# Optimization experiments

Measured on AMD Instinct MI355X. Metric: run time of the kernel, lower is better.

The kernel has to match this reference:

```python
import jax, jax.numpy as jnp
import numpy as np
import math


def _fft_size(n: int) -> int:
    return max(2 * 2 ** int(math.ceil(math.log2(n))), 16)


def setup_inputs() -> dict:
    key = jax.random.key(0)
    k1, k2 = jax.random.split(key)
    b, n, d = 4, 8192, 512
    x = jax.random.normal(k1, (b, n, d), dtype=jnp.float32)
    t = jax.random.normal(k2, (n, d), dtype=jnp.float32)
    return {"x": x, "t": t}


def reference(x, t):
    # x: (b, n, d); t: (n, d) Toeplitz coefficients t0..t_{n-1} per channel.
    # o[b, i, d] = gelu( sum_{j<=i} t[i-j, d] * x[b, j, d] )
    # computed via zero-padded real FFT of size >= 2n (causal linear conv).
    b, n, d = x.shape
    N = _fft_size(n)  # 2 * next_pow2(n)
    t_f = jnp.fft.rfft(t, n=N, axis=0)          # (N//2+1, d) complex
    x_f = jnp.fft.rfft(x, n=N, axis=1)          # (b, N//2+1, d) complex
    y = jnp.fft.irfft(x_f * t_f[None], n=N, axis=1)[:, :n, :]  # (b, n, d)
    return jax.nn.gelu(y)
```

## Files before the change

kernel.cpp:

```cpp
#include <hip/hip_runtime.h>
#include <hip/hip_bf16.h>
#include <math.h>

typedef short short8 __attribute__((ext_vector_type(8)));
typedef float f32x4  __attribute__((ext_vector_type(4)));

#define N_SEQ 8192
#define D_CH  512

__device__ __forceinline__ unsigned short f32_to_bf16_bits(float f) {
    union { float f; unsigned int u; } v; v.f = f;
    unsigned int u = v.u;
    unsigned int r = u + 0x7FFFu + ((u >> 16) & 1u);
    return (unsigned short)(r >> 16);
}

__global__ __launch_bounds__(256) void transpose_cast_kernel(
    const float* __restrict__ x, const float* __restrict__ t,
    unsigned short* __restrict__ xT, unsigned short* __restrict__ tT) {
  __shared__ float tile[64][65];
  int blk = blockIdx.x;
  int bat = blk >> 10;
  int rem = blk & 1023;
  int i0 = (rem >> 3) << 6;
  int d0 = (rem & 7) << 6;
  const float* src; unsigned short* dst;
  if (bat < 4) { src = x + (size_t)bat * N_SEQ * D_CH; dst = xT + (size_t)bat * D_CH * N_SEQ; }
  else         { src = t;                              dst = tT; }
  int tx = threadIdx.x & 63, ty = threadIdx.x >> 6;
  #pragma unroll
  for (int r = ty; r < 64; r += 4)
    tile[r][tx] = src[(size_t)(i0 + r) * D_CH + (d0 + tx)];
  __syncthreads();
  #pragma unroll
  for (int r = ty; r < 64; r += 4)
    dst[(size_t)(d0 + r) * N_SEQ + (i0 + tx)] = f32_to_bf16_bits(tile[tx][r]);
}

__global__ __launch_bounds__(256) void transpose_out_kernel(
    const float* __restrict__ src, float* __restrict__ dst) {
  __shared__ float tile[64][65];
  int blk = blockIdx.x;
  int b   = blk >> 10;
  int rem = blk & 1023;
  int d0 = (rem & 7) << 6;
  int i0 = (rem >> 3) << 6;
  int tx = threadIdx.x & 63, ty = threadIdx.x >> 6;
  #pragma unroll
  for (int r = ty; r < 64; r += 4)
    tile[r][tx] = src[((size_t)(d0 + r) * 4 + b) * N_SEQ + i0 + tx];
  __syncthreads();
  #pragma unroll
  for (int r = ty; r < 64; r += 4)
    dst[((size_t)b * N_SEQ + i0 + r) * D_CH + d0 + tx] = tile[tx][r];
}

constexpr int XLDS_B   = 8192;
constexpr int TSTRIDE  = 272;
constexpr int TLDS_B   = 8 * TSTRIDE;
constexpr int WAVE_LDS = XLDS_B + TLDS_B;

template<int DMAJOR>
__global__ __launch_bounds__(256) void tno_conv_kernel(
    const unsigned short* __restrict__ xT, const unsigned short* __restrict__ tT,
    float* __restrict__ outp) {
  __shared__ __align__(16) char lds_all[4 * WAVE_LDS];
  const int tid  = threadIdx.x;
  const int wv   = tid >> 6;
  const int lane = tid & 63;
  char* ldsX = lds_all + wv * WAVE_LDS;
  char* ldsT = ldsX + XLDS_B;
  const int d = blockIdx.x;

  const int m      = lane & 15;
  const int kb     = (lane >> 4) << 3;
  const int bcol   = m & 3;
  const int sl     = m >> 2;
  const int rA     = m & 7;
  const int aConst = kb - (m & 8);
  const char* tb   = ldsT + rA * TSTRIDE;
  const char* ldsXb = ldsX + (bcol << 4);

  const int sxB   = lane >> 4;
  const int sxRow = (lane & 15) << 1;
  char* ldsXsb = ldsX + (sxB << 4);
  const unsigned short* xTb = xT + (((size_t)sxB * D_CH + d) << 13);

  const int stJ  = lane & 31;
  const int stR0 = (lane >> 5) << 2;
  char* twbase = ldsT + stR0 * TSTRIDE;
  const unsigned short* tTd = tT + ((size_t)d << 13);

  #pragma unroll 1
  for (int region = 0; region < 2; ++region) {
    const int base = (region == 0) ? (wv << 10) : (7168 - (wv << 10));

    f32x4 acc[4][4];
    #pragma unroll
    for (int g = 0; g < 4; ++g)
      #pragma unroll
      for (int k = 0; k < 4; ++k)
        acc[g][k] = (f32x4){0.f, 0.f, 0.f, 0.f};

    auto stage_x_pro = [&](int ls) {
      int row = base - ls + sxRow;
      unsigned int v = 0;
      if (row >= 0) v = *reinterpret_cast<const unsigned int*>(xTb + row);
      int s = row & 1023;
      int byte = ((s >> 3) << 6) | ((s & 7) << 1);
      *reinterpret_cast<unsigned int*>(ldsXsb + byte) = v;
    };
    auto stage_t_pro = [&](int ls) {
      int idx = ls + 64 + stJ;
      unsigned short v = 0;
      if (idx >= 0 && idx < N_SEQ) v = tTd[idx];
      #pragma unroll
      for (int c = 0; c < 4; ++c) {
        int r = stR0 + c;
        int slot = (r - idx) & 127;
        *reinterpret_cast<unsigned short*>(ldsT + r * TSTRIDE + (slot << 1)) = v;
      }
    };
    for (int ls = -992; ls <= -32; ls += 32) stage_x_pro(ls);
    stage_t_pro(-128); stage_t_pro(-96); stage_t_pro(-64);

    int aC = (aConst & 127) << 1;
    short8 af0 = *reinterpret_cast<const short8*>(tb + ((aC + 64) & 255));
    short8 af1 = *reinterpret_cast<const short8*>(tb + ((aC + 32) & 255));

    int xb[4];
    #pragma unroll
    for (int g = 0; g < 4; ++g)
      xb[g] = ((base + ((((g << 2) + sl) << 6) + kb) + 32) & 1023) << 3;

    int xrow = base + sxRow;
    const unsigned short* xp = xTb + xrow;
    int wb; { int s = xrow & 1023; wb = ((s >> 3) << 6) | ((s & 7) << 1); }

    int tidx = 32 + stJ;
    const unsigned short* tp = tTd + tidx;
    int tw0 = ((stR0 + 0 - tidx) & 127) << 1;
    int tw1 = ((stR0 + 1 - tidx) & 127) << 1;
    int tw2 = ((stR0 + 2 - tidx) & 127) << 1;
    int tw3 = ((stR0 + 3 - tidx) & 127) << 1;

#define CONV_ITER(GMIN)                                                         \
  {                                                                             \
    short8 af2 = *reinterpret_cast<const short8*>(tb + aC);                     \
    short8 af3 = *reinterpret_cast<const short8*>(tb + ((aC - 32) & 255));      \
    unsigned int xv = 0;                                                        \
    if (xrow >= 0) xv = *reinterpret_cast<const unsigned int*>(xp);             \
    unsigned int tv = 0;                                                        \
    if (tidx < N_SEQ) tv = (unsigned int)(*tp);                                 \
    _Pragma("unroll")                                                           \
    for (int g = 0; g < 4; ++g) {                                               \
      if (g >= (GMIN)) {                                                        \
        short8 bf = *reinterpret_cast<const short8*>(ldsXb + xb[g]);            \
        acc[g][0] = __builtin_amdgcn_mfma_f32_16x16x32_bf16(af0, bf, acc[g][0], 0, 0, 0); \
        acc[g][1] = __builtin_amdgcn_mfma_f32_16x16x32_bf16(af1, bf, acc[g][1], 0, 0, 0); \
        acc[g][2] = __builtin_amdgcn_mfma_f32_16x16x32_bf16(af2, bf, acc[g][2], 0, 0, 0); \
        acc[g][3] = __builtin_amdgcn_mfma_f32_16x16x32_bf16(af3, bf, acc[g][3], 0, 0, 0); \
        xb[g] = (xb[g] - 256) & 8191;                                           \
      }                                                                         \
    }                                                                           \
    *reinterpret_cast<unsigned int*>(ldsXsb + wb) = xv;                         \
    unsigned short tvs = (unsigned short)tv;                                    \
    *reinterpret_cast<unsigned short*>(twbase + tw0 + 0 * TSTRIDE) = tvs;       \
    *reinterpret_cast<unsigned short*>(twbase + tw1 + 1 * TSTRIDE) = tvs;       \
    *reinterpret_cast<unsigned short*>(twbase + tw2 + 2 * TSTRIDE) = tvs;       \
    *reinterpret_cast<unsigned short*>(twbase + tw3 + 3 * TSTRIDE) = tvs;       \
    af0 = af2; af1 = af3;                                                       \
    aC = (aC - 64) & 255;                                                       \
    xrow -= 32; xp -= 32;                                                       \
    wb = (wb - 256) & 8191;                                                     \
    tidx += 32; tp += 32;                                                       \
    tw0 = (tw0 - 64) & 255; tw1 = (tw1 - 64) & 255;                             \
    tw2 = (tw2 - 64) & 255; tw3 = (tw3 - 64) & 255;                             \
  }

    int l = -32;
    for (; l <= base + 192; l += 32) CONV_ITER(0)
    for (; l <= base + 448; l += 32) CONV_ITER(1)
    for (; l <= base + 704; l += 32) CONV_ITER(2)
    for (; l <= base + 960; l += 32) CONV_ITER(3)
#undef CONV_ITER

    if (DMAJOR) {
      float* op = outp + ((((size_t)d << 2) + bcol) << 13) + base + (sl << 6) + ((lane >> 4) << 2);
      #pragma unroll
      for (int g = 0; g < 4; ++g)
        #pragma unroll
        for (int k = 0; k < 4; ++k)
          #pragma unroll
          for (int r = 0; r < 4; ++r) {
            float v = acc[g][k][r];
            float y = 0.5f * v * (1.f + tanhf(0.79788456080286535588f * (v + 0.044715f * v * v * v)));
            op[(g << 8) + (k << 4) + r] = y;
          }
    } else {
      #pragma unroll
      for (int g = 0; g < 4; ++g)
        #pragma unroll
        for (int k = 0; k < 4; ++k)
          #pragma unroll
          for (int r = 0; r < 4; ++r) {
            int i = base + (((g << 2) + sl) << 6) + (k << 4) + ((lane >> 4) << 2) + r;
            float v = acc[g][k][r];
            float y = 0.5f * v * (1.f + tanhf(0.79788456080286535588f * (v + 0.044715f * v * v * v)));
            outp[(((size_t)bcol << 13) + (size_t)i) * D_CH + d] = y;
          }
    }
  }
}

extern "C" void kernel_launch(void* const* d_in, const int* in_sizes, int n_in,
                              void* d_out, int out_size, void* d_ws, size_t ws_size,
                              hipStream_t stream) {
  const float* x = (const float*)d_in[0];
  const float* t = (const float*)d_in[1];
  float* out = (float*)d_out;

  const size_t xT_elems = (size_t)4 * D_CH * N_SEQ;
  const size_t tT_elems = (size_t)D_CH * N_SEQ;
  unsigned short* xT = (unsigned short*)d_ws;
  unsigned short* tT = xT + xT_elems;
  float* ows = (float*)(tT + tT_elems);
  const size_t need = xT_elems * 2 + tT_elems * 2 + (size_t)4 * N_SEQ * D_CH * 4;
  const bool dmaj = (ws_size >= need);

  hipLaunchKernelGGL(transpose_cast_kernel, dim3(5 * 1024), dim3(256), 0, stream,
                     x, t, xT, tT);
  if (dmaj) {
    hipLaunchKernelGGL((tno_conv_kernel<1>), dim3(D_CH), dim3(256), 0, stream,
                       xT, tT, ows);
    hipLaunchKernelGGL(transpose_out_kernel, dim3(4096), dim3(256), 0, stream,
                       ows, out);
  } else {
    hipLaunchKernelGGL((tno_conv_kernel<0>), dim3(D_CH), dim3(256), 0, stream,
                       xT, tT, out);
  }
}
```

Baseline: 205.7 us.

## Restructure Toeplitz MFMA conv into single-wave blocks with async global-to-LDS x staging

The conv kernel now launches 2048 single-wave blocks (each handling a pair of strips per channel) instead of 512 four-wave blocks. It streams x straight into LDS with global_load_lds using a larger 2048-slot ring, software-pipelines t loads across 8 unrolled iterations, and traverses the strip in reverse order so the partially filled groups come first. It also raises wave priority around the MFMA block and replaces tanhf GELU with an exp2/rcp sigmoid form. The aim is to hide global load latency and spread work over more CUs, at the cost of hand-tuned waitcnt fragility and a slightly different GELU approximation.

```diff
diff --git a/kernel.cpp b/kernel.cpp
--- a/kernel.cpp
+++ b/kernel.cpp
@@ -1,18 +1,30 @@
 #include <hip/hip_runtime.h>
 #include <hip/hip_bf16.h>
-#include <math.h>
 
 typedef short short8 __attribute__((ext_vector_type(8)));
 typedef float f32x4  __attribute__((ext_vector_type(4)));
 
 #define N_SEQ 8192
 #define D_CH  512
+
+constexpr int XSLOTS  = 2048;
+constexpr int XLDS_B  = XSLOTS * 8;
+constexpr int TSTRIDE = 272;
+constexpr int TLDS_B  = 8 * TSTRIDE;
+constexpr int ALL_LDS = XLDS_B + TLDS_B;
 
 __device__ __forceinline__ unsigned short f32_to_bf16_bits(float f) {
     union { float f; unsigned int u; } v; v.f = f;
     unsigned int u = v.u;
     unsigned int r = u + 0x7FFFu + ((u >> 16) & 1u);
     return (unsigned short)(r >> 16);
+}
+
+__device__ __forceinline__ float gelu_f(float v) {
+  float w = v * (2.3022031f + 0.10294296f * v * v);
+  float e = __builtin_amdgcn_exp2f(w);
+  float r = __builtin_amdgcn_rcpf(e + 1.0f);
+  return v - v * r;
 }
 
 __global__ __launch_bounds__(256) void transpose_cast_kernel(
@@ -55,22 +67,15 @@
     dst[((size_t)b * N_SEQ + i0 + r) * D_CH + d0 + tx] = tile[tx][r];
 }
 
-constexpr int XLDS_B   = 8192;
-constexpr int TSTRIDE  = 272;
-constexpr int TLDS_B   = 8 * TSTRIDE;
-constexpr int WAVE_LDS = XLDS_B + TLDS_B;
-
 template<int DMAJOR>
-__global__ __launch_bounds__(256) void tno_conv_kernel(
+__global__ __launch_bounds__(64) void tno_conv_kernel(
     const unsigned short* __restrict__ xT, const unsigned short* __restrict__ tT,
     float* __restrict__ outp) {
-  __shared__ __align__(16) char lds_all[4 * WAVE_LDS];
-  const int tid  = threadIdx.x;
-  const int wv   = tid >> 6;
-  const int lane = tid & 63;
-  char* ldsX = lds_all + wv * WAVE_LDS;
-  char* ldsT = ldsX + XLDS_B;
-  const int d = blockIdx.x;
+  __shared__ __align__(16) char lds[ALL_LDS];
+  const int lane = threadIdx.x & 63;
+  const int blk  = blockIdx.x;
+  const int d    = blk & 511;
+  const int pr   = blk >> 9;
 
   const int m      = lane & 15;
   const int kb     = (lane >> 4) << 3;
@@ -78,22 +83,24 @@
   const int sl     = m >> 2;
   const int rA     = m & 7;
   const int aConst = kb - (m & 8);
-  const char* tb   = ldsT + rA * TSTRIDE;
-  const char* ldsXb = ldsX + (bcol << 4);
-
-  const int sxB   = lane >> 4;
-  const int sxRow = (lane & 15) << 1;
-  char* ldsXsb = ldsX + (sxB << 4);
-  const unsigned short* xTb = xT + (((size_t)sxB * D_CH + d) << 13);
-
+  char* ldsX = lds;
+  char* ldsT = lds + XLDS_B;
+  const char* tb = ldsT + rA * TSTRIDE;
   const int stJ  = lane & 31;
   const int stR0 = (lane >> 5) << 2;
-  char* twbase = ldsT + stR0 * TSTRIDE;
   const unsigned short* tTd = tT + ((size_t)d << 13);
+  const int uLin = (lane & 3) | ((lane >> 4) << 2);
+  const int sb   = (lane >> 2) & 3;
+  const unsigned short* xlaneB = xT + (((size_t)sb * D_CH + d) << 13) + (uLin << 1);
+
+  typedef __attribute__((address_space(3))) unsigned int lds_u32;
+  typedef const __attribute__((address_space(1))) unsigned int glb_u32;
 
   #pragma unroll 1
-  for (int region = 0; region < 2; ++region) {
-    const int base = (region == 0) ? (wv << 10) : (7168 - (wv << 10));
+  for (int si = 0; si < 2; ++si) {
+    const int strip = si ? (7 - pr) : pr;
+    const int base  = strip << 10;
+    const int l_hi  = base + 960;
 
     f32x4 acc[4][4];
     #pragma unroll
@@ -102,87 +109,102 @@
       for (int k = 0; k < 4; ++k)
         acc[g][k] = (f32x4){0.f, 0.f, 0.f, 0.f};
 
-    auto stage_x_pro = [&](int ls) {
-      int row = base - ls + sxRow;
-      unsigned int v = 0;
-      if (row >= 0) v = *reinterpret_cast<const unsigned int*>(xTb + row);
-      int s = row & 1023;
-      int byte = ((s >> 3) << 6) | ((s & 7) << 1);
-      *reinterpret_cast<unsigned int*>(ldsXsb + byte) = v;
-    };
-    auto stage_t_pro = [&](int ls) {
-      int idx = ls + 64 + stJ;
-      unsigned short v = 0;
-      if (idx >= 0 && idx < N_SEQ) v = tTd[idx];
-      #pragma unroll
-      for (int c = 0; c < 4; ++c) {
-        int r = stR0 + c;
-        int slot = (r - idx) & 127;
-        *reinterpret_cast<unsigned short*>(ldsT + r * TSTRIDE + (slot << 1)) = v;
-      }
-    };
-    for (int ls = -992; ls <= -32; ls += 32) stage_x_pro(ls);
-    stage_t_pro(-128); stage_t_pro(-96); stage_t_pro(-64);
-
-    int aC = (aConst & 127) << 1;
-    short8 af0 = *reinterpret_cast<const short8*>(tb + ((aC + 64) & 255));
-    short8 af1 = *reinterpret_cast<const short8*>(tb + ((aC + 32) & 255));
-
-    int xb[4];
+    asm volatile("s_waitcnt vmcnt(0)" ::: "memory");
+
+    unsigned short tp0 = tTd[l_hi + 32 + stJ];
+    unsigned short tp1 = tTd[l_hi + stJ];
+    unsigned short tp2 = tTd[l_hi - 32 + stJ];
+    asm volatile("" ::: "memory");
+
+    #pragma unroll
+    for (int j = 0; j < 30; ++j) {
+      int by = (1088 + 32 * j) << 3;
+      *(unsigned int*)(ldsX + by + (lane << 2)) = 0u;
+    }
+    #pragma unroll
+    for (int j = 0; j < 9; ++j) {
+      int R = 32 * j;
+      __builtin_amdgcn_global_load_lds((glb_u32*)(xlaneB + R),
+                                       (lds_u32*)(ldsX + (R << 3)), 4, 0, 0);
+    }
+    asm volatile("" ::: "memory");
+
+    #pragma unroll
+    for (int c = 0; c < 4; ++c) {
+      int r = stR0 + c;
+      char* cw = ldsT + r * TSTRIDE;
+      *(unsigned short*)(cw + (((r - (l_hi + 32 + stJ)) & 127) << 1)) = tp0;
+      *(unsigned short*)(cw + (((r - (l_hi      + stJ)) & 127) << 1)) = tp1;
+      *(unsigned short*)(cw + (((r - (l_hi - 32 + stJ)) & 127) << 1)) = tp2;
+    }
+
+    unsigned short tv[8];
+    #pragma unroll
+    for (int u = 0; u < 8; ++u)
+      tv[u] = tTd[l_hi - 32 * u - 63 + stJ];
+
+    int aC = ((aConst - l_hi) & 127) << 1;
+    short8 af2 = *(const short8*)(tb + ((aC - 64) & 255));
+    short8 af3 = *(const short8*)(tb + ((aC - 96) & 255));
+    int xo[4];
     #pragma unroll
     for (int g = 0; g < 4; ++g)
-      xb[g] = ((base + ((((g << 2) + sl) << 6) + kb) + 32) & 1023) << 3;
-
-    int xrow = base + sxRow;
-    const unsigned short* xp = xTb + xrow;
-    int wb; { int s = xrow & 1023; wb = ((s >> 3) << 6) | ((s & 7) << 1); }
-
-    int tidx = 32 + stJ;
-    const unsigned short* tp = tTd + tidx;
-    int tw0 = ((stR0 + 0 - tidx) & 127) << 1;
-    int tw1 = ((stR0 + 1 - tidx) & 127) << 1;
-    int tw2 = ((stR0 + 2 - tidx) & 127) << 1;
-    int tw3 = ((stR0 + 3 - tidx) & 127) << 1;
-
-#define CONV_ITER(GMIN)                                                         \
-  {                                                                             \
-    short8 af2 = *reinterpret_cast<const short8*>(tb + aC);                     \
-    short8 af3 = *reinterpret_cast<const short8*>(tb + ((aC - 32) & 255));      \
-    unsigned int xv = 0;                                                        \
-    if (xrow >= 0) xv = *reinterpret_cast<const unsigned int*>(xp);             \
-    unsigned int tv = 0;                                                        \
-    if (tidx < N_SEQ) tv = (unsigned int)(*tp);                                 \
-    _Pragma("unroll")                                                           \
-    for (int g = 0; g < 4; ++g) {                                               \
-      if (g >= (GMIN)) {                                                        \
-        short8 bf = *reinterpret_cast<const short8*>(ldsXb + xb[g]);            \
+      xo[g] = ((((base + ((((g << 2) + sl) << 6) + kb) - l_hi) & 2047) << 3) | (bcol << 4));
+    int twb[4];
+    #pragma unroll
+    for (int c = 0; c < 4; ++c)
+      twb[c] = (((stR0 + c) - (l_hi - 63 + stJ)) & 127) << 1;
+    int tgi = l_hi - 319 + stJ;
+    const unsigned short* xsp = xlaneB + 288;
+    int wb = 288 << 3;
+
+#define CONV_ITER(GMIN, U)                                                       \
+  {                                                                              \
+    asm volatile("s_waitcnt vmcnt(14)" ::: "memory");                            \
+    short8 af0 = *(const short8*)(tb + aC);                                      \
+    short8 af1 = *(const short8*)(tb + ((aC - 32) & 255));                       \
+    __builtin_amdgcn_global_load_lds((glb_u32*)xsp, (lds_u32*)(ldsX + wb), 4, 0, 0); \
+    __builtin_amdgcn_s_setprio(1);                                               \
+    _Pragma("unroll")                                                            \
+    for (int g = 0; g < 4; ++g) {                                                \
+      if (g >= (GMIN)) {                                                         \
+        short8 bf = *(const short8*)(ldsX + xo[g]);                              \
         acc[g][0] = __builtin_amdgcn_mfma_f32_16x16x32_bf16(af0, bf, acc[g][0], 0, 0, 0); \
         acc[g][1] = __builtin_amdgcn_mfma_f32_16x16x32_bf16(af1, bf, acc[g][1], 0, 0, 0); \
         acc[g][2] = __builtin_amdgcn_mfma_f32_16x16x32_bf16(af2, bf, acc[g][2], 0, 0, 0); \
         acc[g][3] = __builtin_amdgcn_mfma_f32_16x16x32_bf16(af3, bf, acc[g][3], 0, 0, 0); \
-        xb[g] = (xb[g] - 256) & 8191;                                           \
-      }                                                                         \
-    }                                                                           \
-    *reinterpret_cast<unsigned int*>(ldsXsb + wb) = xv;                         \
-    unsigned short tvs = (unsigned short)tv;                                    \
-    *reinterpret_cast<unsigned short*>(twbase + tw0 + 0 * TSTRIDE) = tvs;       \
-    *reinterpret_cast<unsigned short*>(twbase + tw1 + 1 * TSTRIDE) = tvs;       \
-    *reinterpret_cast<unsigned short*>(twbase + tw2 + 2 * TSTRIDE) = tvs;       \
-    *reinterpret_cast<unsigned short*>(twbase + tw3 + 3 * TSTRIDE) = tvs;       \
-    af0 = af2; af1 = af3;                                                       \
-    aC = (aC - 64) & 255;                                                       \
-    xrow -= 32; xp -= 32;                                                       \
-    wb = (wb - 256) & 8191;                                                     \
-    tidx += 32; tp += 32;                                                       \
-    tw0 = (tw0 - 64) & 255; tw1 = (tw1 - 64) & 255;                             \
-    tw2 = (tw2 - 64) & 255; tw3 = (tw3 - 64) & 255;                             \
+      }                                                                          \
+      xo[g] = (xo[g] + 256) & 16383;                                             \
+    }                                                                            \
+    __builtin_amdgcn_s_setprio(0);                                               \
+    { unsigned short tvs = tv[U];                                                \
+      _Pragma("unroll")                                                          \
+      for (int c = 0; c < 4; ++c) {                                              \
+        *(unsigned short*)(ldsT + (stR0 + c) * TSTRIDE + twb[c]) = tvs;          \
+        twb[c] = (twb[c] + 64) & 255;                                            \
+      }                                                                          \
+    }                                                                            \
+    { unsigned short v = 0;                                                      \
+      if (tgi >= 0) v = tTd[tgi];                                                \
+      tv[U] = v; tgi -= 32; }                                                    \
+    af2 = af0; af3 = af1;                                                        \
+    aC = (aC + 64) & 255;                                                        \
+    xsp += 32;                                                                   \
+    wb = (wb + 256) & 16383;                                                     \
   }
 
-    int l = -32;
-    for (; l <= base + 192; l += 32) CONV_ITER(0)
-    for (; l <= base + 448; l += 32) CONV_ITER(1)
-    for (; l <= base + 704; l += 32) CONV_ITER(2)
-    for (; l <= base + 960; l += 32) CONV_ITER(3)
+#define PH8(GMIN)                                                                \
+    { _Pragma("unroll")                                                          \
+      for (int u = 0; u < 8; ++u) CONV_ITER(GMIN, u) }
+
+    PH8(3)
+    PH8(2)
+    PH8(1)
+    const int n0 = (strip << 2) + 1;
+    #pragma unroll 1
+    for (int c8 = 0; c8 < n0; ++c8)
+      PH8(0)
+#undef PH8
 #undef CONV_ITER
 
     if (DMAJOR) {
@@ -192,11 +214,8 @@
         #pragma unroll
         for (int k = 0; k < 4; ++k)
           #pragma unroll
-          for (int r = 0; r < 4; ++r) {
-            float v = acc[g][k][r];
-            float y = 0.5f * v * (1.f + tanhf(0.79788456080286535588f * (v + 0.044715f * v * v * v)));
-            op[(g << 8) + (k << 4) + r] = y;
-          }
+          for (int r = 0; r < 4; ++r)
+            op[(g << 8) + (k << 4) + r] = gelu_f(acc[g][k][r]);
     } else {
       #pragma unroll
       for (int g = 0; g < 4; ++g)
@@ -205,9 +224,7 @@
           #pragma unroll
           for (int r = 0; r < 4; ++r) {
             int i = base + (((g << 2) + sl) << 6) + (k << 4) + ((lane >> 4) << 2) + r;
-            float v = acc[g][k][r];
-            float y = 0.5f * v * (1.f + tanhf(0.79788456080286535588f * (v + 0.044715f * v * v * v)));
-            outp[(((size_t)bcol << 13) + (size_t)i) * D_CH + d] = y;
+            outp[(((size_t)bcol << 13) + (size_t)i) * D_CH + d] = gelu_f(acc[g][k][r]);
           }
     }
   }
@@ -231,12 +248,12 @@
   hipLaunchKernelGGL(transpose_cast_kernel, dim3(5 * 1024), dim3(256), 0, stream,
                      x, t, xT, tT);
   if (dmaj) {
-    hipLaunchKernelGGL((tno_conv_kernel<1>), dim3(D_CH), dim3(256), 0, stream,
+    hipLaunchKernelGGL((tno_conv_kernel<1>), dim3(2048), dim3(64), 0, stream,
                        xT, tT, ows);
     hipLaunchKernelGGL(transpose_out_kernel, dim3(4096), dim3(256), 0, stream,
                        ows, out);
   } else {
-    hipLaunchKernelGGL((tno_conv_kernel<0>), dim3(D_CH), dim3(256), 0, stream,
+    hipLaunchKernelGGL((tno_conv_kernel<0>), dim3(2048), dim3(64), 0, stream,
                        xT, tT, out);
   }
 }
```

Result: no change. 202.3 us (-1.7%).
